# Kernel tuning notes

Hardware: AMD Instinct MI355X
Metric: run time of the kernel (lower is better)

The kernel has to match this reference:

```python
import jax, jax.numpy as jnp
import numpy as np

NODE_DIM = 64
EDGE_DIM = 64
HIDDEN = 128
B, N = 2, 512

def setup_inputs() -> dict:
    key = jax.random.key(0)
    ks = jax.random.split(key, 8)
    node_feature = jax.random.normal(ks[0], (B, N, NODE_DIM), dtype=jnp.float32)
    adjacency = (jax.random.uniform(ks[1], (B, N, N)) < 0.1).astype(jnp.float32)
    target_information = jax.random.normal(ks[2], (B, N, NODE_DIM), dtype=jnp.float32)
    edge_feature = jax.random.normal(ks[3], (B, N, N, EDGE_DIM), dtype=jnp.float32)
    node_mask = jnp.ones((B, N), dtype=jnp.float32)
    # edge_fc: Dense(2*node_dim + edge_dim -> hidden) + ReLU
    W_edge = jax.random.normal(ks[4], (2 * NODE_DIM + EDGE_DIM, HIDDEN), dtype=jnp.float32) * 0.05
    b_edge = jnp.zeros((HIDDEN,), dtype=jnp.float32)
    # feature_fc: Dense(hidden + node_dim -> hidden) + ReLU
    W_feat = jax.random.normal(ks[5], (HIDDEN + NODE_DIM, HIDDEN), dtype=jnp.float32) * 0.05
    b_feat = jnp.zeros((HIDDEN,), dtype=jnp.float32)
    return {"node_feature": node_feature, "adjacency": adjacency,
            "target_information": target_information, "edge_feature": edge_feature,
            "node_mask": node_mask, "W_edge": W_edge, "b_edge": b_edge,
            "W_feat": W_feat, "b_feat": b_feat}

def reference(node_feature, adjacency, target_information, edge_feature, node_mask,
              W_edge, b_edge, W_feat, b_feat):
    D = node_feature.shape[-1]
    # concat([node_i, node_j, edge]) @ W_edge == node_i@W1 + node_j@W2 + edge@W3
    # (avoids materializing the [B,N,N,2D+E] concat tensor)
    W1, W2, W3 = W_edge[:D], W_edge[D:2 * D], W_edge[2 * D:]
    hi = jnp.einsum('bnd,dh->bnh', node_feature, W1)   # contribution of node i (rows)
    hj = jnp.einsum('bnd,dh->bnh', node_feature, W2)   # contribution of node j (cols)
    he = jnp.einsum('bije,eh->bijh', edge_feature, W3)  # [B,N,N,H]
    edge_h = jax.nn.relu(hi[:, :, None, :] + hj[:, None, :, :] + he + b_edge)
    # masked sum over neighbors j -> message [B,N,H]
    message = jnp.einsum('bijh,bij->bih', edge_h, adjacency)
    # feature_fc on concat([message, node_feature])
    H = message.shape[-1]
    ending = jax.nn.relu(jnp.einsum('bnh,hk->bnk', message, W_feat[:H])
                         + jnp.einsum('bnd,dk->bnk', node_feature, W_feat[H:])
                         + b_feat)
    return (ending, edge_h, target_information)
```

## Files before the change

kernel.cpp:

```cpp
#include <hip/hip_runtime.h>
#include <hip/hip_bf16.h>

#define NB 2
#define NN 512
#define ND 64
#define NH 128

typedef __attribute__((ext_vector_type(8))) short short8;
typedef __attribute__((ext_vector_type(4))) float f32x4;

__device__ __forceinline__ short f2s(float x) {
    __hip_bfloat16 h = __float2bfloat16(x);
    return *reinterpret_cast<short*>(&h);
}

__device__ __forceinline__ short8 cvt8(const float* p) {
    f32x4 a = *(const f32x4*)p;
    f32x4 b = *(const f32x4*)(p + 4);
    short8 r;
    r[0] = f2s(a[0]); r[1] = f2s(a[1]); r[2] = f2s(a[2]); r[3] = f2s(a[3]);
    r[4] = f2s(b[0]); r[5] = f2s(b[1]); r[6] = f2s(b[2]); r[7] = f2s(b[3]);
    return r;
}

__global__ __launch_bounds__(128) void bias_kernel(
    const float* __restrict__ node,
    const float* __restrict__ W_edge,
    const float* __restrict__ b_edge,
    float* __restrict__ bias)
{
    int bn = blockIdx.x;
    int h = threadIdx.x;
    __shared__ float nrow[ND];
    if (h < ND) nrow[h] = node[bn * ND + h];
    __syncthreads();
    float acc = b_edge[h];
    #pragma unroll
    for (int d = 0; d < ND; d++)
        acc += nrow[d] * W_edge[d * NH + h];
    bias[bn * NH + h] = acc;
}

__global__ __launch_bounds__(256) void edge_kernel(
    const float* __restrict__ ef,
    const float* __restrict__ node,
    const float* __restrict__ adj,
    const float* __restrict__ W_edge,
    const float* __restrict__ bias,
    float* __restrict__ edge_out,
    float* __restrict__ message)
{
    constexpr int BTS = NH + 8;
    __shared__ short BT[NH * BTS];
    __shared__ float msgbuf[4][NH];

    int blk = blockIdx.x;
    int b = blk >> 9;
    int tid = threadIdx.x;

    for (int t = tid; t < NH * NH; t += 256) {
        int h = t >> 7;
        int k = t & 127;
        int row = (k < ND) ? (2 * ND + k) : k;
        BT[h * BTS + k] = f2s(W_edge[row * NH + h]);
    }
    __syncthreads();

    int lane = tid & 63;
    int wave = tid >> 6;
    int m = lane & 15;
    int quad = lane >> 4;

    float bias_l[8];
    #pragma unroll
    for (int ht = 0; ht < 8; ht++)
        bias_l[ht] = bias[blk * NH + ht * 16 + m];

    float msg_l[8] = {0.f, 0.f, 0.f, 0.f, 0.f, 0.f, 0.f, 0.f};

    const float* adjrow = adj + (size_t)blk * NN;
    float* outbase = edge_out + (size_t)blk * NN * NH;

    for (int c = 0; c < 8; c++) {
        int j0 = wave * 128 + c * 16;
        int jm = j0 + m;
        const float* efp = ef + ((size_t)blk * NN + jm) * ND;
        const float* ndp = node + ((size_t)b * NN + jm) * ND;
        short8 af[4];
        af[0] = cvt8(efp + quad * 8);
        af[1] = cvt8(efp + 32 + quad * 8);
        af[2] = cvt8(ndp + quad * 8);
        af[3] = cvt8(ndp + 32 + quad * 8);

        float av[4];
        #pragma unroll
        for (int r = 0; r < 4; r++)
            av[r] = adjrow[j0 + quad * 4 + r];

        #pragma unroll
        for (int ht = 0; ht < 8; ht++) {
            f32x4 acc = {0.f, 0.f, 0.f, 0.f};
            const short* bt = BT + (ht * 16 + m) * BTS;
            #pragma unroll
            for (int kf = 0; kf < 4; kf++) {
                short8 bfr = *(const short8*)(bt + kf * 32 + quad * 8);
                acc = __builtin_amdgcn_mfma_f32_16x16x32_bf16(af[kf], bfr, acc, 0, 0, 0);
            }
            int h = ht * 16 + m;
            float bsum = bias_l[ht];
            #pragma unroll
            for (int r = 0; r < 4; r++) {
                float v = acc[r] + bsum;
                v = fmaxf(v, 0.f);
                int j = j0 + quad * 4 + r;
                outbase[(size_t)j * NH + h] = v;
                msg_l[ht] += av[r] * v;
            }
        }
    }

    #pragma unroll
    for (int ht = 0; ht < 8; ht++) {
        float v = msg_l[ht];
        v += __shfl_xor(v, 16, 64);
        v += __shfl_xor(v, 32, 64);
        if (quad == 0) msgbuf[wave][ht * 16 + m] = v;
    }
    __syncthreads();
    if (tid < NH) {
        float s = msgbuf[0][tid] + msgbuf[1][tid] + msgbuf[2][tid] + msgbuf[3][tid];
        message[(size_t)blk * NH + tid] = s;
    }
}

__global__ __launch_bounds__(128) void out_kernel(
    const float* __restrict__ node,
    const float* __restrict__ message,
    const float* __restrict__ W_feat,
    const float* __restrict__ b_feat,
    float* __restrict__ ending)
{
    int bn = blockIdx.x;
    int k = threadIdx.x;
    __shared__ float mrow[NH];
    __shared__ float nrow[ND];
    mrow[k] = message[(size_t)bn * NH + k];
    if (k < ND) nrow[k] = node[bn * ND + k];
    __syncthreads();
    float acc = b_feat[k];
    #pragma unroll 4
    for (int h = 0; h < NH; h++)
        acc += mrow[h] * W_feat[h * NH + k];
    #pragma unroll 4
    for (int d = 0; d < ND; d++)
        acc += nrow[d] * W_feat[(NH + d) * NH + k];
    ending[(size_t)bn * NH + k] = fmaxf(acc, 0.f);
}

extern "C" void kernel_launch(void* const* d_in, const int* in_sizes, int n_in,
                              void* d_out, int out_size, void* d_ws, size_t ws_size,
                              hipStream_t stream)
{
    const float* node   = (const float*)d_in[0];
    const float* adj    = (const float*)d_in[1];
    const float* tgt    = (const float*)d_in[2];
    const float* ef     = (const float*)d_in[3];
    const float* W_edge = (const float*)d_in[5];
    const float* b_edge = (const float*)d_in[6];
    const float* W_feat = (const float*)d_in[7];
    const float* b_feat = (const float*)d_in[8];

    float* out_ending = (float*)d_out;
    float* out_edge   = out_ending + (size_t)NB * NN * NH;
    float* out_tgt    = out_edge + (size_t)NB * NN * NN * NH;

    float* bias    = (float*)d_ws;
    float* message = bias + (size_t)NB * NN * NH;

    bias_kernel<<<NB * NN, NH, 0, stream>>>(node, W_edge, b_edge, bias);
    edge_kernel<<<NB * NN, 256, 0, stream>>>(ef, node, adj, W_edge, bias, out_edge, message);
    out_kernel<<<NB * NN, NH, 0, stream>>>(node, message, W_feat, b_feat, out_ending);
    hipMemcpyAsync(out_tgt, tgt, (size_t)NB * NN * ND * sizeof(float),
                   hipMemcpyDeviceToDevice, stream);
}
```

Before: 442.3 us.

## Precompute node projections and swap MFMA operands for vectorized edge output stores

The node_j projection is now precomputed in the pre-kernel (hjb, with bias folded in), and the node_i projection is stored as hi. The edge kernel's MFMA contraction therefore drops from K=128 to K=64, and node-j features are no longer converted to bf16. The MFMA operands are swapped so weights are the A operand, held in registers, and edge features are B. Each lane then owns one j row and writes 4 contiguous floats per store, where it previously issued scattered scalar stores. In exchange, the kernel reads an extra 128-float hj row per j from global memory, does a longer message reduction with 32 accumulators, and may face register pressure under the occupancy hint of 3.

```diff
diff --git a/kernel.cpp b/kernel.cpp
--- a/kernel.cpp
+++ b/kernel.cpp
@@ -23,113 +23,119 @@
     return r;
 }
 
-__global__ __launch_bounds__(128) void bias_kernel(
+__global__ __launch_bounds__(128) void pre_kernel(
     const float* __restrict__ node,
     const float* __restrict__ W_edge,
     const float* __restrict__ b_edge,
-    float* __restrict__ bias)
+    float* __restrict__ hi,
+    float* __restrict__ hjb)
 {
     int bn = blockIdx.x;
     int h = threadIdx.x;
     __shared__ float nrow[ND];
     if (h < ND) nrow[h] = node[bn * ND + h];
     __syncthreads();
-    float acc = b_edge[h];
-    #pragma unroll
-    for (int d = 0; d < ND; d++)
-        acc += nrow[d] * W_edge[d * NH + h];
-    bias[bn * NH + h] = acc;
+    float a1 = 0.f, a2 = b_edge[h];
+    #pragma unroll 4
+    for (int d = 0; d < ND; d++) {
+        float nd = nrow[d];
+        a1 += nd * W_edge[d * NH + h];
+        a2 += nd * W_edge[(ND + d) * NH + h];
+    }
+    hi[bn * NH + h] = a1;
+    hjb[bn * NH + h] = a2;
 }
 
-__global__ __launch_bounds__(256) void edge_kernel(
+__global__ __launch_bounds__(256, 3) void edge_kernel(
     const float* __restrict__ ef,
-    const float* __restrict__ node,
     const float* __restrict__ adj,
     const float* __restrict__ W_edge,
-    const float* __restrict__ bias,
+    const float* __restrict__ hi,
+    const float* __restrict__ hjb,
     float* __restrict__ edge_out,
     float* __restrict__ message)
 {
-    constexpr int BTS = NH + 8;
-    __shared__ short BT[NH * BTS];
+    constexpr int WTS = ND + 8;
+    __shared__ short WT[NH * WTS];
     __shared__ float msgbuf[4][NH];
 
     int blk = blockIdx.x;
     int b = blk >> 9;
     int tid = threadIdx.x;
 
-    for (int t = tid; t < NH * NH; t += 256) {
-        int h = t >> 7;
-        int k = t & 127;
-        int row = (k < ND) ? (2 * ND + k) : k;
-        BT[h * BTS + k] = f2s(W_edge[row * NH + h]);
+    for (int t = tid; t < NH * ND; t += 256) {
+        int h = t >> 6;
+        int k = t & 63;
+        WT[h * WTS + k] = f2s(W_edge[(2 * ND + k) * NH + h]);
     }
     __syncthreads();
 
     int lane = tid & 63;
     int wave = tid >> 6;
-    int m = lane & 15;
+    int n = lane & 15;
     int quad = lane >> 4;
 
-    float bias_l[8];
+    short8 wf[16];
+    #pragma unroll
+    for (int ht = 0; ht < 8; ht++) {
+        #pragma unroll
+        for (int kf = 0; kf < 2; kf++)
+            wf[ht * 2 + kf] = *(const short8*)(WT + (ht * 16 + n) * WTS + kf * 32 + quad * 8);
+    }
+
+    f32x4 hi_l[8];
     #pragma unroll
     for (int ht = 0; ht < 8; ht++)
-        bias_l[ht] = bias[blk * NH + ht * 16 + m];
+        hi_l[ht] = *(const f32x4*)(hi + blk * NH + ht * 16 + quad * 4);
 
-    float msg_l[8] = {0.f, 0.f, 0.f, 0.f, 0.f, 0.f, 0.f, 0.f};
+    float msg[32];
+    #pragma unroll
+    for (int i = 0; i < 32; i++) msg[i] = 0.f;
 
     const float* adjrow = adj + (size_t)blk * NN;
     float* outbase = edge_out + (size_t)blk * NN * NH;
 
     for (int c = 0; c < 8; c++) {
-        int j0 = wave * 128 + c * 16;
-        int jm = j0 + m;
-        const float* efp = ef + ((size_t)blk * NN + jm) * ND;
-        const float* ndp = node + ((size_t)b * NN + jm) * ND;
-        short8 af[4];
-        af[0] = cvt8(efp + quad * 8);
-        af[1] = cvt8(efp + 32 + quad * 8);
-        af[2] = cvt8(ndp + quad * 8);
-        af[3] = cvt8(ndp + 32 + quad * 8);
-
-        float av[4];
-        #pragma unroll
-        for (int r = 0; r < 4; r++)
-            av[r] = adjrow[j0 + quad * 4 + r];
+        int jn = wave * 128 + c * 16 + n;
+        const float* efp = ef + ((size_t)blk * NN + jn) * ND;
+        short8 af0 = cvt8(efp + quad * 8);
+        short8 af1 = cvt8(efp + 32 + quad * 8);
+        float aj = adjrow[jn];
+        const float* hjp = hjb + ((size_t)b * NN + jn) * NH;
+        float* outp = outbase + (size_t)jn * NH;
 
         #pragma unroll
         for (int ht = 0; ht < 8; ht++) {
             f32x4 acc = {0.f, 0.f, 0.f, 0.f};
-            const short* bt = BT + (ht * 16 + m) * BTS;
-            #pragma unroll
-            for (int kf = 0; kf < 4; kf++) {
-                short8 bfr = *(const short8*)(bt + kf * 32 + quad * 8);
-                acc = __builtin_amdgcn_mfma_f32_16x16x32_bf16(af[kf], bfr, acc, 0, 0, 0);
-            }
-            int h = ht * 16 + m;
-            float bsum = bias_l[ht];
+            acc = __builtin_amdgcn_mfma_f32_16x16x32_bf16(wf[ht * 2 + 0], af0, acc, 0, 0, 0);
+            acc = __builtin_amdgcn_mfma_f32_16x16x32_bf16(wf[ht * 2 + 1], af1, acc, 0, 0, 0);
+            f32x4 hjv = *(const f32x4*)(hjp + ht * 16 + quad * 4);
+            f32x4 hiv = hi_l[ht];
+            f32x4 outv;
             #pragma unroll
             for (int r = 0; r < 4; r++) {
-                float v = acc[r] + bsum;
+                float v = acc[r] + hiv[r] + hjv[r];
                 v = fmaxf(v, 0.f);
-                int j = j0 + quad * 4 + r;
-                outbase[(size_t)j * NH + h] = v;
-                msg_l[ht] += av[r] * v;
+                outv[r] = v;
+                msg[ht * 4 + r] += aj * v;
             }
+            *(f32x4*)(outp + ht * 16 + quad * 4) = outv;
         }
     }
 
     #pragma unroll
-    for (int ht = 0; ht < 8; ht++) {
-        float v = msg_l[ht];
-        v += __shfl_xor(v, 16, 64);
-        v += __shfl_xor(v, 32, 64);
-        if (quad == 0) msgbuf[wave][ht * 16 + m] = v;
+    for (int i = 0; i < 32; i++) {
+        float v = msg[i];
+        v += __shfl_xor(v, 1, 64);
+        v += __shfl_xor(v, 2, 64);
+        v += __shfl_xor(v, 4, 64);
+        v += __shfl_xor(v, 8, 64);
+        if (n == 0) msgbuf[wave][(i >> 2) * 16 + quad * 4 + (i & 3)] = v;
     }
     __syncthreads();
     if (tid < NH) {
-        float s = msgbuf[0][tid] + msgbuf[1][tid] + msgbuf[2][tid] + msgbuf[3][tid];
-        message[(size_t)blk * NH + tid] = s;
+        message[(size_t)blk * NH + tid] =
+            msgbuf[0][tid] + msgbuf[1][tid] + msgbuf[2][tid] + msgbuf[3][tid];
     }
 }
 
@@ -174,11 +180,12 @@
     float* out_edge   = out_ending + (size_t)NB * NN * NH;
     float* out_tgt    = out_edge + (size_t)NB * NN * NN * NH;
 
-    float* bias    = (float*)d_ws;
-    float* message = bias + (size_t)NB * NN * NH;
+    float* hi      = (float*)d_ws;
+    float* hjb     = hi + (size_t)NB * NN * NH;
+    float* message = hjb + (size_t)NB * NN * NH;
 
-    bias_kernel<<<NB * NN, NH, 0, stream>>>(node, W_edge, b_edge, bias);
-    edge_kernel<<<NB * NN, 256, 0, stream>>>(ef, node, adj, W_edge, bias, out_edge, message);
+    pre_kernel<<<NB * NN, NH, 0, stream>>>(node, W_edge, b_edge, hi, hjb);
+    edge_kernel<<<NB * NN, 256, 0, stream>>>(ef, adj, W_edge, hi, hjb, out_edge, message);
     out_kernel<<<NB * NN, NH, 0, stream>>>(node, message, W_feat, b_feat, out_ending);
     hipMemcpyAsync(out_tgt, tgt, (size_t)NB * NN * ND * sizeof(float),
                    hipMemcpyDeviceToDevice, stream);
```

Result: slower. 587.3 us (+32.8%).
